# Optimization experiments

Hardware: AMD Instinct MI355X
Metric: run time of the kernel (lower is better)

Reference implementation:

```python
import jax, jax.numpy as jnp
import numpy as np

N, D, E, R = 50000, 128, 640000, 500
BN_EPS = 1e-3  # keras BatchNormalization default
L2_EPS = 1e-12  # tf.nn.l2_normalize default


def setup_inputs() -> dict:
    key = jax.random.key(0)
    ks = jax.random.split(key, 10)
    rows = jnp.sort(jax.random.randint(ks[0], (E,), 0, N, dtype=jnp.int32))
    cols = jax.random.randint(ks[1], (E,), 0, N, dtype=jnp.int32)
    return {
        "x": jax.random.normal(ks[2], (N, D), dtype=jnp.float32),
        "rows": rows,
        "cols": cols,
        "adj_vals": jax.random.uniform(ks[3], (E,), dtype=jnp.float32),
        "rel_ids": jax.random.randint(ks[4], (E,), 0, R, dtype=jnp.int32),
        "gamma1": jnp.ones((D,), jnp.float32),
        "beta1": jnp.zeros((D,), jnp.float32),
        "mean1": jnp.zeros((D,), jnp.float32),
        "var1": jnp.ones((D,), jnp.float32),
        "W1": jax.random.normal(ks[5], (D, D), dtype=jnp.float32) * 0.05,
        "b1": jnp.zeros((D,), jnp.float32),
        "gamma2": jnp.ones((D,), jnp.float32),
        "beta2": jnp.zeros((D,), jnp.float32),
        "mean2": jnp.zeros((D,), jnp.float32),
        "var2": jnp.ones((D,), jnp.float32),
        "relation_coeffs": jax.random.uniform(ks[6], (R,), dtype=jnp.float32),
        "coeff_kernel": jax.random.normal(ks[7], (N, 1), dtype=jnp.float32) * 0.05,
        "Wd": jax.random.normal(ks[8], (D, D), dtype=jnp.float32) * 0.05,
        "bd": jnp.zeros((D,), jnp.float32),
    }


def _bn(h, gamma, beta, mean, var):
    # keras BatchNormalization, inference mode (moving stats)
    return (h - mean) * jax.lax.rsqrt(var + BN_EPS) * gamma + beta


def _spmm(vals, rows, cols, h, n):
    # sparse [n,n] @ dense [n,d]: gather source rows, weight, scatter-add to dest
    return jax.ops.segment_sum(vals[:, None] * h[cols], rows, num_segments=n)


def _l2n(a):
    # tf.nn.l2_normalize(a, axis=1)
    sq = jnp.sum(a * a, axis=1, keepdims=True)
    return a * jax.lax.rsqrt(jnp.maximum(sq, L2_EPS))


def reference(x, rows, cols, adj_vals, rel_ids,
              gamma1, beta1, mean1, var1, W1, b1,
              gamma2, beta2, mean2, var2,
              relation_coeffs, coeff_kernel, Wd, bd):
    n = x.shape[0]
    # ---- agg1: alinet_gcn: tanh(A @ (BN(x) @ W1) + b1) ----
    h = _bn(x, gamma1, beta1, mean1, var1)
    y1 = jnp.tanh(_spmm(adj_vals, rows, cols, h @ W1, n) + b1)
    # ---- agg2: Rgin ----
    h2 = _bn(y1, gamma2, beta2, mean2, var2)
    # relation-weighted edge values: A.values / (rel_coeffs[values] + 1)
    ev = adj_vals / (relation_coeffs[rel_ids] + 1.0)
    agg = _spmm(ev, rows, cols, h2, n)
    self_term = h2 * (coeff_kernel + 1.0)  # CoeffLayer(mul=True)
    y2 = (agg + self_term) @ Wd + bd       # Dense(dim)
    # ---- output: concat of per-layer l2-normalized embeddings, renormalized ----
    y = jnp.concatenate([_l2n(x), _l2n(y1), _l2n(y2)], axis=1)
    return _l2n(y)
```

## Files before the change

kernel.cpp:

```cpp
#include <hip/hip_runtime.h>
#include <math.h>

#define D 128
#define BN_EPS 1e-3f
#define L2_EPS 1e-12f

typedef unsigned int uint;
typedef unsigned short ushort;
typedef __attribute__((ext_vector_type(8))) short bf16x8;
typedef __attribute__((ext_vector_type(4))) float f32x4;

__device__ __forceinline__ ushort f2bf(float f) {
  uint u = __float_as_uint(f);
  uint r = (u + 0x7fffu + ((u >> 16) & 1u)) >> 16;
  return (ushort)r;
}
__device__ __forceinline__ float bflo(uint u) { return __uint_as_float(u << 16); }
__device__ __forceinline__ float bfhi(uint u) { return __uint_as_float(u & 0xffff0000u); }
__device__ __forceinline__ float bf2f(ushort h) { return __uint_as_float(((uint)h) << 16); }

__device__ __forceinline__ void pack_bfrag_block(
    const float* __restrict__ W, const float* __restrict__ gamma,
    const float* __restrict__ var, ushort* __restrict__ Bf, int blk, int tid) {
  int t = blk * 256 + tid;
  int f = t >> 6, lane = t & 63;
  int kc = f >> 3, nt = f & 7, q = lane >> 4, m = lane & 15;
  ushort tmp[8];
#pragma unroll
  for (int j = 0; j < 8; ++j) {
    int k = kc * 32 + q * 8 + j;
    float s = gamma[k] * rsqrtf(var[k] + BN_EPS);
    tmp[j] = f2bf(s * W[k * D + nt * 16 + m]);
  }
  uint4 o;
  o.x = (uint)tmp[0] | ((uint)tmp[1] << 16);
  o.y = (uint)tmp[2] | ((uint)tmp[3] << 16);
  o.z = (uint)tmp[4] | ((uint)tmp[5] << 16);
  o.w = (uint)tmp[6] | ((uint)tmp[7] << 16);
  reinterpret_cast<uint4*>(Bf)[t] = o;
}

__device__ __forceinline__ void bn_bias_block(
    const float* __restrict__ W, const float* __restrict__ gamma,
    const float* __restrict__ beta, const float* __restrict__ mean,
    const float* __restrict__ var, float* __restrict__ outb, int j) {
  float acc = 0.f;
  for (int k = 0; k < D; ++k) {
    float s = gamma[k] * rsqrtf(var[k] + BN_EPS);
    float sh = beta[k] - mean[k] * s;
    acc += sh * W[k * D + j];
  }
  outb[j] = acc;
}

__global__ __launch_bounds__(256) void prep_kernel(
    const float* __restrict__ x, ushort* __restrict__ xbf, int n4,
    const int* __restrict__ rows, int* __restrict__ row_ptr, int n, int e,
    const float* __restrict__ W1, const float* __restrict__ g1,
    const float* __restrict__ v1, ushort* __restrict__ Bf1,
    const float* __restrict__ Wd, const float* __restrict__ g2,
    const float* __restrict__ v2, ushort* __restrict__ Bf2,
    const float* __restrict__ beta1, const float* __restrict__ mean1,
    float* __restrict__ bnb,
    const float* __restrict__ beta2, const float* __restrict__ mean2,
    float* __restrict__ shd,
    const int* __restrict__ cols, const float* __restrict__ adj,
    const int* __restrict__ rel, const float* __restrict__ relc,
    uint2* __restrict__ ew1, uint2* __restrict__ ew2,
    int nbConv, int nbRp) {
  const int b = blockIdx.x, tid = threadIdx.x;
  if (b < nbConv) {
    int i = b * 256 + tid;
    if (i < n4) {
      float4 v = reinterpret_cast<const float4*>(x)[i];
      ushort4 o;
      o.x = f2bf(v.x); o.y = f2bf(v.y); o.z = f2bf(v.z); o.w = f2bf(v.w);
      reinterpret_cast<ushort4*>(xbf)[i] = o;
    }
    return;
  }
  int bb = b - nbConv;
  if (bb < nbRp) {
    int i = bb * 256 + tid;
    if (i <= n) {
      int lo = 0, hi = e;
      while (lo < hi) {
        int mid = (lo + hi) >> 1;
        if (rows[mid] < i) lo = mid + 1; else hi = mid;
      }
      row_ptr[i] = lo;
    }
    return;
  }
  bb -= nbRp;
  if (bb < 8) { pack_bfrag_block(W1, g1, v1, Bf1, bb, tid); return; }
  if (bb < 16) { pack_bfrag_block(Wd, g2, v2, Bf2, bb - 8, tid); return; }
  if (bb == 16) { if (tid < D) bn_bias_block(W1, g1, beta1, mean1, v1, bnb, tid); return; }
  if (bb == 17) { if (tid < D) bn_bias_block(Wd, g2, beta2, mean2, v2, shd, tid); return; }
  int i = (bb - 18) * 256 + tid;
  if (i < e) {
    uint c = (uint)cols[i];
    float a = adj[i];
    ew1[i] = make_uint2(c, __float_as_uint(a));
    float w2 = a / (relc[rel[i]] + 1.0f);
    ew2[i] = make_uint2(c, __float_as_uint(w2));
  } else if (i == e) {
    ew1[i] = make_uint2(0u, 0u);
    ew2[i] = make_uint2(0u, 0u);
  }
}

template <bool SELF>
__global__ __launch_bounds__(256) void spmm4_kernel(
    const ushort* __restrict__ src, const int* __restrict__ row_ptr,
    const uint2* __restrict__ ew, const float* __restrict__ ck,
    ushort* __restrict__ outA, float* __restrict__ rowsum, int n) {
  const int lane = threadIdx.x & 63;
  const int g = lane >> 4, m = lane & 15;
  const int r = blockIdx.x * 16 + (threadIdx.x >> 6) * 4 + g;
  const int rr = r < n ? r : n - 1;
  const int e0 = row_ptr[rr];
  int len = row_ptr[rr + 1] - e0;
  if (r >= n) len = 0;
  int mx = len;
  mx = max(mx, __shfl_xor(mx, 16));
  mx = max(mx, __shfl_xor(mx, 32));
  const int lastOff = len > 0 ? len - 1 : 0;

  const uint4* S4 = reinterpret_cast<const uint4*>(src);
  float acc[8] = {0.f, 0.f, 0.f, 0.f, 0.f, 0.f, 0.f, 0.f};
  float ws = 0.f;

  for (int i = 0; i < mx; i += 4) {
    uint2 md[4];
    uint4 gv[4];
#pragma unroll
    for (int u = 0; u < 4; ++u) {
      int ii = i + u;
      int off = ii < len ? ii : lastOff;
      md[u] = ew[e0 + off];
    }
#pragma unroll
    for (int u = 0; u < 4; ++u) gv[u] = S4[(size_t)md[u].x * 16 + m];
#pragma unroll
    for (int u = 0; u < 4; ++u) {
      float w = (i + u) < len ? __uint_as_float(md[u].y) : 0.f;
      ws += w;
      acc[0] = fmaf(w, bflo(gv[u].x), acc[0]);
      acc[1] = fmaf(w, bfhi(gv[u].x), acc[1]);
      acc[2] = fmaf(w, bflo(gv[u].y), acc[2]);
      acc[3] = fmaf(w, bfhi(gv[u].y), acc[3]);
      acc[4] = fmaf(w, bflo(gv[u].z), acc[4]);
      acc[5] = fmaf(w, bfhi(gv[u].z), acc[5]);
      acc[6] = fmaf(w, bflo(gv[u].w), acc[6]);
      acc[7] = fmaf(w, bfhi(gv[u].w), acc[7]);
    }
  }

  if (r >= n) return;
  if (SELF) {
    uint4 us = S4[(size_t)rr * 16 + m];
    float cp = ck[rr] + 1.0f;
    acc[0] = fmaf(cp, bflo(us.x), acc[0]);
    acc[1] = fmaf(cp, bfhi(us.x), acc[1]);
    acc[2] = fmaf(cp, bflo(us.y), acc[2]);
    acc[3] = fmaf(cp, bfhi(us.y), acc[3]);
    acc[4] = fmaf(cp, bflo(us.z), acc[4]);
    acc[5] = fmaf(cp, bfhi(us.z), acc[5]);
    acc[6] = fmaf(cp, bflo(us.w), acc[6]);
    acc[7] = fmaf(cp, bfhi(us.w), acc[7]);
  }
  uint4 o;
  o.x = (uint)f2bf(acc[0]) | ((uint)f2bf(acc[1]) << 16);
  o.y = (uint)f2bf(acc[2]) | ((uint)f2bf(acc[3]) << 16);
  o.z = (uint)f2bf(acc[4]) | ((uint)f2bf(acc[5]) << 16);
  o.w = (uint)f2bf(acc[6]) | ((uint)f2bf(acc[7]) << 16);
  reinterpret_cast<uint4*>(outA)[(size_t)r * 16 + m] = o;
  if (m == 0) rowsum[r] = ws;
}

__global__ __launch_bounds__(256) void gemm1_mfma_kernel(
    const ushort* __restrict__ A, const ushort* __restrict__ Bf,
    const float* __restrict__ bnb, const float* __restrict__ b1,
    const float* __restrict__ rs1, ushort* __restrict__ y1, int M) {
  const int wave = threadIdx.x >> 6, lane = threadIdx.x & 63;
  const int row0 = blockIdx.x * 64 + wave * 16;
  if (row0 >= M) return;
  const int m = lane & 15, q = lane >> 4;
  const int row = row0 + m;
  const int arow = row < M ? row : M - 1;

  const bf16x8* Av = reinterpret_cast<const bf16x8*>(A);
  const bf16x8* Bv = reinterpret_cast<const bf16x8*>(Bf);

  bf16x8 af[4];
#pragma unroll
  for (int kc = 0; kc < 4; ++kc) af[kc] = Av[(size_t)arow * 16 + kc * 4 + q];

  f32x4 acc[8];
#pragma unroll
  for (int nt = 0; nt < 8; ++nt) acc[nt] = (f32x4){0.f, 0.f, 0.f, 0.f};

#pragma unroll
  for (int kc = 0; kc < 4; ++kc) {
#pragma unroll
    for (int nt = 0; nt < 8; ++nt) {
      bf16x8 b = Bv[(kc * 8 + nt) * 64 + lane];
      acc[nt] = __builtin_amdgcn_mfma_f32_16x16x32_bf16(b, af[kc], acc[nt], 0, 0, 0);
    }
  }

  if (row < M) {
    float rs = rs1[row];
#pragma unroll
    for (int nt = 0; nt < 8; ++nt) {
      const float4 bn = *reinterpret_cast<const float4*>(&bnb[nt * 16 + q * 4]);
      const float4 bb = *reinterpret_cast<const float4*>(&b1[nt * 16 + q * 4]);
      ushort4 o;
      o.x = f2bf(tanhf(acc[nt][0] + rs * bn.x + bb.x));
      o.y = f2bf(tanhf(acc[nt][1] + rs * bn.y + bb.y));
      o.z = f2bf(tanhf(acc[nt][2] + rs * bn.z + bb.z));
      o.w = f2bf(tanhf(acc[nt][3] + rs * bn.w + bb.w));
      *reinterpret_cast<ushort4*>(&y1[(size_t)row * D + nt * 16 + q * 4]) = o;
    }
  }
}

__global__ __launch_bounds__(256) void gemm2_fused_kernel(
    const ushort* __restrict__ A2, const ushort* __restrict__ Bf,
    const float* __restrict__ shd, const float* __restrict__ bd,
    const float* __restrict__ rs2, const float* __restrict__ ck,
    const float* __restrict__ x, const ushort* __restrict__ y1,
    float* __restrict__ out, int M) {
  const int wave = threadIdx.x >> 6, lane = threadIdx.x & 63;
  const int row0 = blockIdx.x * 64 + wave * 16;
  if (row0 >= M) return;
  const int m = lane & 15, q = lane >> 4;
  const int row = row0 + m;
  const int arow = row < M ? row : M - 1;

  const bf16x8* Av = reinterpret_cast<const bf16x8*>(A2);
  const bf16x8* Bv = reinterpret_cast<const bf16x8*>(Bf);

  bf16x8 af[4];
#pragma unroll
  for (int kc = 0; kc < 4; ++kc) af[kc] = Av[(size_t)arow * 16 + kc * 4 + q];

  f32x4 acc[8];
#pragma unroll
  for (int nt = 0; nt < 8; ++nt) acc[nt] = (f32x4){0.f, 0.f, 0.f, 0.f};

#pragma unroll
  for (int kc = 0; kc < 4; ++kc) {
#pragma unroll
    for (int nt = 0; nt < 8; ++nt) {
      bf16x8 b = Bv[(kc * 8 + nt) * 64 + lane];
      acc[nt] = __builtin_amdgcn_mfma_f32_16x16x32_bf16(b, af[kc], acc[nt], 0, 0, 0);
    }
  }

  const float rb = rs2[arow] + ck[arow] + 1.0f;
  float4 xv[8];
  ushort4 y1v[8];
  float s0 = 0.f, s1 = 0.f, s2 = 0.f;
#pragma unroll
  for (int nt = 0; nt < 8; ++nt) {
    const float4 sh = *reinterpret_cast<const float4*>(&shd[nt * 16 + q * 4]);
    const float4 bb = *reinterpret_cast<const float4*>(&bd[nt * 16 + q * 4]);
    acc[nt][0] += rb * sh.x + bb.x;
    acc[nt][1] += rb * sh.y + bb.y;
    acc[nt][2] += rb * sh.z + bb.z;
    acc[nt][3] += rb * sh.w + bb.w;
    s2 += acc[nt][0] * acc[nt][0] + acc[nt][1] * acc[nt][1] +
          acc[nt][2] * acc[nt][2] + acc[nt][3] * acc[nt][3];
    xv[nt] = *reinterpret_cast<const float4*>(&x[(size_t)arow * D + nt * 16 + q * 4]);
    s0 += xv[nt].x * xv[nt].x + xv[nt].y * xv[nt].y +
          xv[nt].z * xv[nt].z + xv[nt].w * xv[nt].w;
    y1v[nt] = *reinterpret_cast<const ushort4*>(&y1[(size_t)arow * D + nt * 16 + q * 4]);
    float ya = bf2f(y1v[nt].x), yb = bf2f(y1v[nt].y);
    float yc = bf2f(y1v[nt].z), yd = bf2f(y1v[nt].w);
    s1 += ya * ya + yb * yb + yc * yc + yd * yd;
  }
  s0 += __shfl_xor(s0, 16); s0 += __shfl_xor(s0, 32);
  s1 += __shfl_xor(s1, 16); s1 += __shfl_xor(s1, 32);
  s2 += __shfl_xor(s2, 16); s2 += __shfl_xor(s2, 32);
  const float i0 = 1.0f / sqrtf(fmaxf(s0, L2_EPS));
  const float i1 = 1.0f / sqrtf(fmaxf(s1, L2_EPS));
  const float i2 = 1.0f / sqrtf(fmaxf(s2, L2_EPS));
  const float tot = s0 * i0 * i0 + s1 * i1 * i1 + s2 * i2 * i2;
  const float sc = 1.0f / sqrtf(fmaxf(tot, L2_EPS));
  const float f0 = i0 * sc, f1 = i1 * sc, f2 = i2 * sc;

  if (row < M) {
    float* orow = out + (size_t)row * 384;
#pragma unroll
    for (int nt = 0; nt < 8; ++nt) {
      const int c = nt * 16 + q * 4;
      float4 ox = make_float4(xv[nt].x * f0, xv[nt].y * f0, xv[nt].z * f0, xv[nt].w * f0);
      float4 oy = make_float4(bf2f(y1v[nt].x) * f1, bf2f(y1v[nt].y) * f1,
                              bf2f(y1v[nt].z) * f1, bf2f(y1v[nt].w) * f1);
      float4 oz = make_float4(acc[nt][0] * f2, acc[nt][1] * f2,
                              acc[nt][2] * f2, acc[nt][3] * f2);
      *reinterpret_cast<float4*>(orow + c) = ox;
      *reinterpret_cast<float4*>(orow + 128 + c) = oy;
      *reinterpret_cast<float4*>(orow + 256 + c) = oz;
    }
  }
}

extern "C" void kernel_launch(void* const* d_in, const int* in_sizes, int n_in,
                              void* d_out, int out_size, void* d_ws, size_t ws_size,
                              hipStream_t stream) {
  const float* x      = (const float*)d_in[0];
  const int*   rows   = (const int*)d_in[1];
  const int*   cols   = (const int*)d_in[2];
  const float* adj    = (const float*)d_in[3];
  const int*   rel    = (const int*)d_in[4];
  const float* gamma1 = (const float*)d_in[5];
  const float* beta1  = (const float*)d_in[6];
  const float* mean1  = (const float*)d_in[7];
  const float* var1   = (const float*)d_in[8];
  const float* W1     = (const float*)d_in[9];
  const float* b1     = (const float*)d_in[10];
  const float* gamma2 = (const float*)d_in[11];
  const float* beta2  = (const float*)d_in[12];
  const float* mean2  = (const float*)d_in[13];
  const float* var2   = (const float*)d_in[14];
  const float* relc   = (const float*)d_in[15];
  const float* ck     = (const float*)d_in[16];
  const float* Wd     = (const float*)d_in[17];
  const float* bd     = (const float*)d_in[18];
  float* out = (float*)d_out;

  const int n = in_sizes[0] / D;
  const int e = in_sizes[1];
  size_t nd = (size_t)n * D;

  char* p = (char*)d_ws;
  ushort* xbf   = (ushort*)p; p += nd * 2;
  ushort* y1bf  = (ushort*)p; p += nd * 2;
  ushort* aggbf = (ushort*)p; p += nd * 2;
  ushort* Bf1   = (ushort*)p; p += 32768;
  ushort* Bf2   = (ushort*)p; p += 32768;
  float*  bnb   = (float*)p;  p += 512;
  float*  shd   = (float*)p;  p += 512;
  float*  rs1   = (float*)p;  p += (size_t)n * 4;
  float*  rs2   = (float*)p;  p += (size_t)n * 4;
  p = (char*)(((uintptr_t)p + 15) & ~(uintptr_t)15);
  uint2* ew1    = (uint2*)p;  p += (size_t)(e + 1) * 8;
  uint2* ew2    = (uint2*)p;  p += (size_t)(e + 1) * 8;
  int* row_ptr  = (int*)p;    p += (size_t)(n + 1) * 4;

  const int n4 = (int)(nd / 4);
  const int nbConv = (n4 + 255) / 256;
  const int nbRp = (n + 1 + 255) / 256;
  const int nbEw = (e + 1 + 255) / 256;
  const int nbPrep = nbConv + nbRp + 18 + nbEw;

  prep_kernel<<<nbPrep, 256, 0, stream>>>(
      x, xbf, n4, rows, row_ptr, n, e,
      W1, gamma1, var1, Bf1, Wd, gamma2, var2, Bf2,
      beta1, mean1, bnb, beta2, mean2, shd,
      cols, adj, rel, relc, ew1, ew2, nbConv, nbRp);

  int sblocks = (n + 15) / 16;
  int gblocks = (n + 63) / 64;

  spmm4_kernel<false><<<sblocks, 256, 0, stream>>>(
      xbf, row_ptr, ew1, nullptr, aggbf, rs1, n);
  gemm1_mfma_kernel<<<gblocks, 256, 0, stream>>>(aggbf, Bf1, bnb, b1, rs1, y1bf, n);
  spmm4_kernel<true><<<sblocks, 256, 0, stream>>>(
      y1bf, row_ptr, ew2, ck, aggbf, rs2, n);
  gemm2_fused_kernel<<<gblocks, 256, 0, stream>>>(
      aggbf, Bf2, shd, bd, rs2, ck, x, y1bf, out, n);
}
```

Baseline: 231.4 us.

## Fuse SpMM with following MFMA GEMM via shared-memory tiles

Merges each SpMM kernel with its dense GEMM kernel, so the aggregated 16-row tile is packed to bf16 in LDS and consumed by MFMA directly, and each wave computes 2 of the 8 output column tiles. This removes the global aggregate buffer, the row-sum arrays and two launches. Output and y1 writes are staged through padded shared memory so stores to global memory are coalesced. The cost is extra __syncthreads and redundant B-fragment loads per 16-row block, since each block now reloads weight fragments for only 16 rows.

```diff
diff --git a/kernel.cpp b/kernel.cpp
--- a/kernel.cpp
+++ b/kernel.cpp
@@ -4,6 +4,8 @@
 #define D 128
 #define BN_EPS 1e-3f
 #define L2_EPS 1e-12f
+#define AGG_S 136
+#define OUT_S 392
 
 typedef unsigned int uint;
 typedef unsigned short ushort;
@@ -111,13 +113,10 @@
 }
 
 template <bool SELF>
-__global__ __launch_bounds__(256) void spmm4_kernel(
-    const ushort* __restrict__ src, const int* __restrict__ row_ptr,
+__device__ __forceinline__ float spmm_rows(
+    const uint4* __restrict__ S4, const int* __restrict__ row_ptr,
     const uint2* __restrict__ ew, const float* __restrict__ ck,
-    ushort* __restrict__ outA, float* __restrict__ rowsum, int n) {
-  const int lane = threadIdx.x & 63;
-  const int g = lane >> 4, m = lane & 15;
-  const int r = blockIdx.x * 16 + (threadIdx.x >> 6) * 4 + g;
+    int r, int n, int m, float acc[8]) {
   const int rr = r < n ? r : n - 1;
   const int e0 = row_ptr[rr];
   int len = row_ptr[rr + 1] - e0;
@@ -127,8 +126,8 @@
   mx = max(mx, __shfl_xor(mx, 32));
   const int lastOff = len > 0 ? len - 1 : 0;
 
-  const uint4* S4 = reinterpret_cast<const uint4*>(src);
-  float acc[8] = {0.f, 0.f, 0.f, 0.f, 0.f, 0.f, 0.f, 0.f};
+#pragma unroll
+  for (int j = 0; j < 8; ++j) acc[j] = 0.f;
   float ws = 0.f;
 
   for (int i = 0; i < mx; i += 4) {
@@ -157,8 +156,7 @@
     }
   }
 
-  if (r >= n) return;
-  if (SELF) {
+  if (SELF && r < n) {
     uint4 us = S4[(size_t)rr * 16 + m];
     float cp = ck[rr] + 1.0f;
     acc[0] = fmaf(cp, bflo(us.x), acc[0]);
@@ -170,120 +168,161 @@
     acc[6] = fmaf(cp, bflo(us.w), acc[6]);
     acc[7] = fmaf(cp, bfhi(us.w), acc[7]);
   }
+  return ws;
+}
+
+__device__ __forceinline__ uint4 pack_acc(const float acc[8]) {
   uint4 o;
   o.x = (uint)f2bf(acc[0]) | ((uint)f2bf(acc[1]) << 16);
   o.y = (uint)f2bf(acc[2]) | ((uint)f2bf(acc[3]) << 16);
   o.z = (uint)f2bf(acc[4]) | ((uint)f2bf(acc[5]) << 16);
   o.w = (uint)f2bf(acc[6]) | ((uint)f2bf(acc[7]) << 16);
-  reinterpret_cast<uint4*>(outA)[(size_t)r * 16 + m] = o;
-  if (m == 0) rowsum[r] = ws;
-}
-
-__global__ __launch_bounds__(256) void gemm1_mfma_kernel(
-    const ushort* __restrict__ A, const ushort* __restrict__ Bf,
+  return o;
+}
+
+__global__ __launch_bounds__(256) void spmm_gemm1_kernel(
+    const ushort* __restrict__ src, const int* __restrict__ row_ptr,
+    const uint2* __restrict__ ew, const ushort* __restrict__ Bf,
     const float* __restrict__ bnb, const float* __restrict__ b1,
-    const float* __restrict__ rs1, ushort* __restrict__ y1, int M) {
-  const int wave = threadIdx.x >> 6, lane = threadIdx.x & 63;
-  const int row0 = blockIdx.x * 64 + wave * 16;
-  if (row0 >= M) return;
-  const int m = lane & 15, q = lane >> 4;
-  const int row = row0 + m;
-  const int arow = row < M ? row : M - 1;
-
-  const bf16x8* Av = reinterpret_cast<const bf16x8*>(A);
+    ushort* __restrict__ y1, int n) {
+  __shared__ ushort aggT[16 * AGG_S];
+  __shared__ ushort y1T[16 * AGG_S];
+  __shared__ float rsL[16];
+
+  const int tid = threadIdx.x;
+  const int wave = tid >> 6, lane = tid & 63;
+  const int g = lane >> 4, m = lane & 15;
+  const int rloc = wave * 4 + g;
+  const int r = blockIdx.x * 16 + rloc;
+
+  float acc[8];
+  float ws = spmm_rows<false>(reinterpret_cast<const uint4*>(src), row_ptr,
+                              ew, nullptr, r, n, m, acc);
+  *reinterpret_cast<uint4*>(&aggT[rloc * AGG_S + m * 8]) = pack_acc(acc);
+  if (m == 0) rsL[rloc] = ws;
+  __syncthreads();
+
   const bf16x8* Bv = reinterpret_cast<const bf16x8*>(Bf);
-
   bf16x8 af[4];
 #pragma unroll
-  for (int kc = 0; kc < 4; ++kc) af[kc] = Av[(size_t)arow * 16 + kc * 4 + q];
-
-  f32x4 acc[8];
-#pragma unroll
-  for (int nt = 0; nt < 8; ++nt) acc[nt] = (f32x4){0.f, 0.f, 0.f, 0.f};
-
+  for (int kc = 0; kc < 4; ++kc)
+    af[kc] = *reinterpret_cast<const bf16x8*>(&aggT[m * AGG_S + kc * 32 + g * 8]);
+
+  f32x4 acc2[2];
+  acc2[0] = (f32x4){0.f, 0.f, 0.f, 0.f};
+  acc2[1] = (f32x4){0.f, 0.f, 0.f, 0.f};
+  const int nt0 = wave * 2;
 #pragma unroll
   for (int kc = 0; kc < 4; ++kc) {
 #pragma unroll
-    for (int nt = 0; nt < 8; ++nt) {
-      bf16x8 b = Bv[(kc * 8 + nt) * 64 + lane];
-      acc[nt] = __builtin_amdgcn_mfma_f32_16x16x32_bf16(b, af[kc], acc[nt], 0, 0, 0);
-    }
-  }
-
-  if (row < M) {
-    float rs = rs1[row];
-#pragma unroll
-    for (int nt = 0; nt < 8; ++nt) {
-      const float4 bn = *reinterpret_cast<const float4*>(&bnb[nt * 16 + q * 4]);
-      const float4 bb = *reinterpret_cast<const float4*>(&b1[nt * 16 + q * 4]);
-      ushort4 o;
-      o.x = f2bf(tanhf(acc[nt][0] + rs * bn.x + bb.x));
-      o.y = f2bf(tanhf(acc[nt][1] + rs * bn.y + bb.y));
-      o.z = f2bf(tanhf(acc[nt][2] + rs * bn.z + bb.z));
-      o.w = f2bf(tanhf(acc[nt][3] + rs * bn.w + bb.w));
-      *reinterpret_cast<ushort4*>(&y1[(size_t)row * D + nt * 16 + q * 4]) = o;
-    }
-  }
-}
-
-__global__ __launch_bounds__(256) void gemm2_fused_kernel(
-    const ushort* __restrict__ A2, const ushort* __restrict__ Bf,
+    for (int t = 0; t < 2; ++t) {
+      bf16x8 b = Bv[(kc * 8 + nt0 + t) * 64 + lane];
+      acc2[t] = __builtin_amdgcn_mfma_f32_16x16x32_bf16(b, af[kc], acc2[t], 0, 0, 0);
+    }
+  }
+
+  const float rs = rsL[m];
+#pragma unroll
+  for (int t = 0; t < 2; ++t) {
+    const int c = (nt0 + t) * 16 + g * 4;
+    const float4 bn = *reinterpret_cast<const float4*>(&bnb[c]);
+    const float4 bb = *reinterpret_cast<const float4*>(&b1[c]);
+    ushort4 ov;
+    ov.x = f2bf(tanhf(acc2[t][0] + rs * bn.x + bb.x));
+    ov.y = f2bf(tanhf(acc2[t][1] + rs * bn.y + bb.y));
+    ov.z = f2bf(tanhf(acc2[t][2] + rs * bn.z + bb.z));
+    ov.w = f2bf(tanhf(acc2[t][3] + rs * bn.w + bb.w));
+    *reinterpret_cast<ushort4*>(&y1T[m * AGG_S + c]) = ov;
+  }
+  __syncthreads();
+
+  const int row = tid >> 4, col = tid & 15;
+  uint4 v = *reinterpret_cast<const uint4*>(&y1T[row * AGG_S + col * 8]);
+  const size_t gi = (size_t)blockIdx.x * 256 + tid;
+  if ((int)(gi >> 4) < n) reinterpret_cast<uint4*>(y1)[gi] = v;
+}
+
+__global__ __launch_bounds__(256) void spmm_gemm2_kernel(
+    const ushort* __restrict__ src , const int* __restrict__ row_ptr,
+    const uint2* __restrict__ ew, const ushort* __restrict__ Bf,
     const float* __restrict__ shd, const float* __restrict__ bd,
-    const float* __restrict__ rs2, const float* __restrict__ ck,
-    const float* __restrict__ x, const ushort* __restrict__ y1,
-    float* __restrict__ out, int M) {
-  const int wave = threadIdx.x >> 6, lane = threadIdx.x & 63;
-  const int row0 = blockIdx.x * 64 + wave * 16;
-  if (row0 >= M) return;
-  const int m = lane & 15, q = lane >> 4;
-  const int row = row0 + m;
-  const int arow = row < M ? row : M - 1;
-
-  const bf16x8* Av = reinterpret_cast<const bf16x8*>(A2);
+    const float* __restrict__ ck, const float* __restrict__ x,
+    float* __restrict__ out, int n) {
+  __shared__ __align__(16) char smemRaw[16 * OUT_S * 4];
+  __shared__ float rsL[16];
+  __shared__ float sp0[4][16], sp1[4][16], sp2[4][16];
+  ushort* aggT = reinterpret_cast<ushort*>(smemRaw);
+  float* outT = reinterpret_cast<float*>(smemRaw);
+
+  const int tid = threadIdx.x;
+  const int wave = tid >> 6, lane = tid & 63;
+  const int g = lane >> 4, m = lane & 15;
+  const int rloc = wave * 4 + g;
+  const int r = blockIdx.x * 16 + rloc;
+
+  float acc[8];
+  float ws = spmm_rows<true>(reinterpret_cast<const uint4*>(src), row_ptr,
+                             ew, ck, r, n, m, acc);
+  *reinterpret_cast<uint4*>(&aggT[rloc * AGG_S + m * 8]) = pack_acc(acc);
+  if (m == 0) rsL[rloc] = ws;
+  __syncthreads();
+
   const bf16x8* Bv = reinterpret_cast<const bf16x8*>(Bf);
-
   bf16x8 af[4];
 #pragma unroll
-  for (int kc = 0; kc < 4; ++kc) af[kc] = Av[(size_t)arow * 16 + kc * 4 + q];
-
-  f32x4 acc[8];
-#pragma unroll
-  for (int nt = 0; nt < 8; ++nt) acc[nt] = (f32x4){0.f, 0.f, 0.f, 0.f};
-
+  for (int kc = 0; kc < 4; ++kc)
+    af[kc] = *reinterpret_cast<const bf16x8*>(&aggT[m * AGG_S + kc * 32 + g * 8]);
+
+  f32x4 acc2[2];
+  acc2[0] = (f32x4){0.f, 0.f, 0.f, 0.f};
+  acc2[1] = (f32x4){0.f, 0.f, 0.f, 0.f};
+  const int nt0 = wave * 2;
 #pragma unroll
   for (int kc = 0; kc < 4; ++kc) {
 #pragma unroll
-    for (int nt = 0; nt < 8; ++nt) {
-      bf16x8 b = Bv[(kc * 8 + nt) * 64 + lane];
-      acc[nt] = __builtin_amdgcn_mfma_f32_16x16x32_bf16(b, af[kc], acc[nt], 0, 0, 0);
-    }
-  }
-
-  const float rb = rs2[arow] + ck[arow] + 1.0f;
-  float4 xv[8];
-  ushort4 y1v[8];
-  float s0 = 0.f, s1 = 0.f, s2 = 0.f;
-#pragma unroll
-  for (int nt = 0; nt < 8; ++nt) {
-    const float4 sh = *reinterpret_cast<const float4*>(&shd[nt * 16 + q * 4]);
-    const float4 bb = *reinterpret_cast<const float4*>(&bd[nt * 16 + q * 4]);
-    acc[nt][0] += rb * sh.x + bb.x;
-    acc[nt][1] += rb * sh.y + bb.y;
-    acc[nt][2] += rb * sh.z + bb.z;
-    acc[nt][3] += rb * sh.w + bb.w;
-    s2 += acc[nt][0] * acc[nt][0] + acc[nt][1] * acc[nt][1] +
-          acc[nt][2] * acc[nt][2] + acc[nt][3] * acc[nt][3];
-    xv[nt] = *reinterpret_cast<const float4*>(&x[(size_t)arow * D + nt * 16 + q * 4]);
-    s0 += xv[nt].x * xv[nt].x + xv[nt].y * xv[nt].y +
-          xv[nt].z * xv[nt].z + xv[nt].w * xv[nt].w;
-    y1v[nt] = *reinterpret_cast<const ushort4*>(&y1[(size_t)arow * D + nt * 16 + q * 4]);
-    float ya = bf2f(y1v[nt].x), yb = bf2f(y1v[nt].y);
-    float yc = bf2f(y1v[nt].z), yd = bf2f(y1v[nt].w);
-    s1 += ya * ya + yb * yb + yc * yc + yd * yd;
-  }
-  s0 += __shfl_xor(s0, 16); s0 += __shfl_xor(s0, 32);
-  s1 += __shfl_xor(s1, 16); s1 += __shfl_xor(s1, 32);
-  s2 += __shfl_xor(s2, 16); s2 += __shfl_xor(s2, 32);
+    for (int t = 0; t < 2; ++t) {
+      bf16x8 b = Bv[(kc * 8 + nt0 + t) * 64 + lane];
+      acc2[t] = __builtin_amdgcn_mfma_f32_16x16x32_bf16(b, af[kc], acc2[t], 0, 0, 0);
+    }
+  }
+
+  const int rm = min(blockIdx.x * 16 + m, n - 1);
+  const int c0 = wave * 32 + g * 8;
+  const float4 xv0 = *reinterpret_cast<const float4*>(&x[(size_t)rm * D + c0]);
+  const float4 xv1 = *reinterpret_cast<const float4*>(&x[(size_t)rm * D + c0 + 4]);
+  const uint4 yv = *reinterpret_cast<const uint4*>(&src[(size_t)rm * D + c0]);
+  const float ya = bflo(yv.x), yb = bfhi(yv.x), yc = bflo(yv.y), yd = bfhi(yv.y);
+  const float ye = bflo(yv.z), yf = bfhi(yv.z), yg = bflo(yv.w), yh = bfhi(yv.w);
+
+  float s0p = xv0.x * xv0.x + xv0.y * xv0.y + xv0.z * xv0.z + xv0.w * xv0.w +
+              xv1.x * xv1.x + xv1.y * xv1.y + xv1.z * xv1.z + xv1.w * xv1.w;
+  float s1p = ya * ya + yb * yb + yc * yc + yd * yd +
+              ye * ye + yf * yf + yg * yg + yh * yh;
+
+  const float rbias = rsL[m] + ck[rm] + 1.0f;
+  float s2p = 0.f;
+#pragma unroll
+  for (int t = 0; t < 2; ++t) {
+    const int c = (nt0 + t) * 16 + g * 4;
+    const float4 sh = *reinterpret_cast<const float4*>(&shd[c]);
+    const float4 bb = *reinterpret_cast<const float4*>(&bd[c]);
+    acc2[t][0] += rbias * sh.x + bb.x;
+    acc2[t][1] += rbias * sh.y + bb.y;
+    acc2[t][2] += rbias * sh.z + bb.z;
+    acc2[t][3] += rbias * sh.w + bb.w;
+    s2p += acc2[t][0] * acc2[t][0] + acc2[t][1] * acc2[t][1] +
+           acc2[t][2] * acc2[t][2] + acc2[t][3] * acc2[t][3];
+  }
+
+  s0p += __shfl_xor(s0p, 16); s0p += __shfl_xor(s0p, 32);
+  s1p += __shfl_xor(s1p, 16); s1p += __shfl_xor(s1p, 32);
+  s2p += __shfl_xor(s2p, 16); s2p += __shfl_xor(s2p, 32);
+  if (lane < 16) { sp0[wave][lane] = s0p; sp1[wave][lane] = s1p; sp2[wave][lane] = s2p; }
+  __syncthreads();
+
+  const float s0 = sp0[0][m] + sp0[1][m] + sp0[2][m] + sp0[3][m];
+  const float s1 = sp1[0][m] + sp1[1][m] + sp1[2][m] + sp1[3][m];
+  const float s2 = sp2[0][m] + sp2[1][m] + sp2[2][m] + sp2[3][m];
   const float i0 = 1.0f / sqrtf(fmaxf(s0, L2_EPS));
   const float i1 = 1.0f / sqrtf(fmaxf(s1, L2_EPS));
   const float i2 = 1.0f / sqrtf(fmaxf(s2, L2_EPS));
@@ -291,20 +330,30 @@
   const float sc = 1.0f / sqrtf(fmaxf(tot, L2_EPS));
   const float f0 = i0 * sc, f1 = i1 * sc, f2 = i2 * sc;
 
-  if (row < M) {
-    float* orow = out + (size_t)row * 384;
-#pragma unroll
-    for (int nt = 0; nt < 8; ++nt) {
-      const int c = nt * 16 + q * 4;
-      float4 ox = make_float4(xv[nt].x * f0, xv[nt].y * f0, xv[nt].z * f0, xv[nt].w * f0);
-      float4 oy = make_float4(bf2f(y1v[nt].x) * f1, bf2f(y1v[nt].y) * f1,
-                              bf2f(y1v[nt].z) * f1, bf2f(y1v[nt].w) * f1);
-      float4 oz = make_float4(acc[nt][0] * f2, acc[nt][1] * f2,
-                              acc[nt][2] * f2, acc[nt][3] * f2);
-      *reinterpret_cast<float4*>(orow + c) = ox;
-      *reinterpret_cast<float4*>(orow + 128 + c) = oy;
-      *reinterpret_cast<float4*>(orow + 256 + c) = oz;
-    }
+  float* orow = &outT[m * OUT_S];
+  *reinterpret_cast<float4*>(&orow[c0]) =
+      make_float4(xv0.x * f0, xv0.y * f0, xv0.z * f0, xv0.w * f0);
+  *reinterpret_cast<float4*>(&orow[c0 + 4]) =
+      make_float4(xv1.x * f0, xv1.y * f0, xv1.z * f0, xv1.w * f0);
+  *reinterpret_cast<float4*>(&orow[128 + c0]) =
+      make_float4(ya * f1, yb * f1, yc * f1, yd * f1);
+  *reinterpret_cast<float4*>(&orow[128 + c0 + 4]) =
+      make_float4(ye * f1, yf * f1, yg * f1, yh * f1);
+#pragma unroll
+  for (int t = 0; t < 2; ++t) {
+    const int c = (nt0 + t) * 16 + g * 4;
+    *reinterpret_cast<float4*>(&orow[256 + c]) =
+        make_float4(acc2[t][0] * f2, acc2[t][1] * f2, acc2[t][2] * f2, acc2[t][3] * f2);
+  }
+  __syncthreads();
+
+#pragma unroll
+  for (int it = 0; it < 6; ++it) {
+    const int idx = it * 256 + tid;
+    const int rw = idx / 96, cc = idx % 96;
+    float4 v = *reinterpret_cast<const float4*>(&outT[rw * OUT_S + cc * 4]);
+    const int gr = blockIdx.x * 16 + rw;
+    if (gr < n) reinterpret_cast<float4*>(out)[(size_t)gr * 96 + cc] = v;
   }
 }
 
@@ -339,13 +388,10 @@
   char* p = (char*)d_ws;
   ushort* xbf   = (ushort*)p; p += nd * 2;
   ushort* y1bf  = (ushort*)p; p += nd * 2;
-  ushort* aggbf = (ushort*)p; p += nd * 2;
   ushort* Bf1   = (ushort*)p; p += 32768;
   ushort* Bf2   = (ushort*)p; p += 32768;
   float*  bnb   = (float*)p;  p += 512;
   float*  shd   = (float*)p;  p += 512;
-  float*  rs1   = (float*)p;  p += (size_t)n * 4;
-  float*  rs2   = (float*)p;  p += (size_t)n * 4;
   p = (char*)(((uintptr_t)p + 15) & ~(uintptr_t)15);
   uint2* ew1    = (uint2*)p;  p += (size_t)(e + 1) * 8;
   uint2* ew2    = (uint2*)p;  p += (size_t)(e + 1) * 8;
@@ -363,14 +409,9 @@
       beta1, mean1, bnb, beta2, mean2, shd,
       cols, adj, rel, relc, ew1, ew2, nbConv, nbRp);
 
-  int sblocks = (n + 15) / 16;
-  int gblocks = (n + 63) / 64;
-
-  spmm4_kernel<false><<<sblocks, 256, 0, stream>>>(
-      xbf, row_ptr, ew1, nullptr, aggbf, rs1, n);
-  gemm1_mfma_kernel<<<gblocks, 256, 0, stream>>>(aggbf, Bf1, bnb, b1, rs1, y1bf, n);
-  spmm4_kernel<true><<<sblocks, 256, 0, stream>>>(
-      y1bf, row_ptr, ew2, ck, aggbf, rs2, n);
-  gemm2_fused_kernel<<<gblocks, 256, 0, stream>>>(
-      aggbf, Bf2, shd, bd, rs2, ck, x, y1bf, out, n);
-}
+  const int fblocks = (n + 15) / 16;
+  spmm_gemm1_kernel<<<fblocks, 256, 0, stream>>>(
+      xbf, row_ptr, ew1, Bf1, bnb, b1, y1bf, n);
+  spmm_gemm2_kernel<<<fblocks, 256, 0, stream>>>(
+      y1bf, row_ptr, ew2, Bf2, shd, bd, ck, x, out, n);
+}
```

After: 214.3 us. -7.4%, faster.
